# Performance work log

Hardware: AMD Instinct MI355X
Metric: run time of the kernel (lower is better)

Reference implementation:

```python
import jax, jax.numpy as jnp
import numpy as np

DIM_IN = 1024
DIM_K = 64
EPS = 1e-5

def setup_inputs() -> dict:
    key = jax.random.key(0)
    ks = jax.random.split(key, 9)
    s_in = 1.0 / np.sqrt(DIM_IN)
    s_k = 1.0 / np.sqrt(DIM_K)
    return {
        "X": jax.random.normal(ks[0], (8, 2048, DIM_IN), dtype=jnp.float32),
        "Wq": jax.random.uniform(ks[1], (DIM_IN, DIM_K), jnp.float32, -s_in, s_in),
        "bq": jax.random.uniform(ks[2], (DIM_K,), jnp.float32, -s_in, s_in),
        "Wk": jax.random.uniform(ks[3], (DIM_IN, DIM_K), jnp.float32, -s_in, s_in),
        "bk": jax.random.uniform(ks[4], (DIM_K,), jnp.float32, -s_in, s_in),
        "Wv": jax.random.uniform(ks[5], (DIM_IN, DIM_K), jnp.float32, -s_in, s_in),
        "bv": jax.random.uniform(ks[6], (DIM_K,), jnp.float32, -s_in, s_in),
        "Wo": jax.random.uniform(ks[7], (DIM_K, DIM_IN), jnp.float32, -s_k, s_k),
        "bo": jax.random.uniform(ks[8], (DIM_IN,), jnp.float32, -s_k, s_k),
        "gamma": jnp.ones((DIM_IN,), jnp.float32),
        "beta": jnp.zeros((DIM_IN,), jnp.float32),
    }

def reference(X, Wq, bq, Wk, bk, Wv, bv, Wo, bo, gamma, beta):
    q = X @ Wq + bq                       # [B,S,K]
    k = X @ Wk + bk
    v = X @ Wv + bv
    scores = jnp.einsum("bqk,bsk->bqs", q, k) / jnp.sqrt(jnp.float32(DIM_K))
    attn = jax.nn.softmax(scores, axis=2)  # [B,S,S]
    av = jnp.einsum("bqs,bsk->bqk", attn, v)
    y = X + av @ Wo + bo                  # residual, [B,S,D]
    mu = jnp.mean(y, axis=-1, keepdims=True)
    var = jnp.mean(jnp.square(y - mu), axis=-1, keepdims=True)
    return (y - mu) / jnp.sqrt(var + EPS) * gamma + beta
```

## Files before the change

kernel.cpp:

```cpp
#include <hip/hip_runtime.h>
#include <hip/hip_bf16.h>

#define DIM_D 1024
#define DIM_KH 64
#define SEQ   2048
#define BATCH 8
#define NROWS (BATCH*SEQ)
#define KVSPLIT 4
#define KEYS_PER_SPLIT (SEQ/KVSPLIT)

typedef __attribute__((ext_vector_type(8))) short short8;
typedef __attribute__((ext_vector_type(4))) short short4v;
typedef __attribute__((ext_vector_type(4))) float floatx4;

__device__ __forceinline__ ushort f2bf(float f) {
    union { __hip_bfloat16 h; ushort u; } cv;
    cv.h = __float2bfloat16(f);
    return cv.u;
}

__device__ __forceinline__ uint4 pack8(float4 a, float4 b) {
    uint4 p;
    p.x = (uint)f2bf(a.x) | ((uint)f2bf(a.y) << 16);
    p.y = (uint)f2bf(a.z) | ((uint)f2bf(a.w) << 16);
    p.z = (uint)f2bf(b.x) | ((uint)f2bf(b.y) << 16);
    p.w = (uint)f2bf(b.z) | ((uint)f2bf(b.w) << 16);
    return p;
}

__global__ void wcvt_kernel(const float* __restrict__ Wq,
                            const float* __restrict__ Wk,
                            const float* __restrict__ Wv,
                            ushort* __restrict__ WT)
{
    const int n  = blockIdx.x;
    const int o  = n >> 6;
    const int nn = n & 63;
    const float* W = (o == 0) ? Wq : (o == 1) ? Wk : Wv;
    #pragma unroll
    for (int i = 0; i < 4; i++) {
        int k = threadIdx.x + i * 256;
        WT[(size_t)n * DIM_D + k] = f2bf(W[(size_t)k * DIM_KH + nn]);
    }
}

__global__ void wocvt_kernel(const float* __restrict__ Wo, ushort* __restrict__ WoT)
{
    const int tid = threadIdx.x;
    const int n = blockIdx.x * 4 + (tid >> 6);
    const int k = tid & 63;
    WoT[(size_t)n * DIM_KH + k] = f2bf(Wo[(size_t)k * DIM_D + n]);
}

__global__ __launch_bounds__(256, 1) void qkv_mfma(
    const float* __restrict__ X, const ushort* __restrict__ WT,
    const float* __restrict__ bq, const float* __restrict__ bk,
    const float* __restrict__ bv,
    ushort* __restrict__ Qb, ushort* __restrict__ Kb, ushort* __restrict__ Vb)
{
    const int tid = threadIdx.x;
    const int m0  = blockIdx.x * 64;
    const int o   = blockIdx.y;

    __shared__ ushort Xs[2][64 * 64];
    __shared__ ushort Wls[2][64 * 64];

    const int w  = tid >> 6;
    const int l  = tid & 63;
    const int ql = l & 15;
    const int g  = (l >> 4) & 3;
    const int swz = (ql & 7) << 3;

    const int sr  = tid >> 2;
    const int sc  = (tid & 3) << 4;
    const int ssw = (sr & 7) << 3;
    const float*  Xrow = X  + (size_t)(m0 + sr) * DIM_D + sc;
    const ushort* Wrow = WT + (size_t)(o * 64 + sr) * DIM_D + sc;

    float4 xr[4];
    uint4  wr[2];

    floatx4 acc[4];
    #pragma unroll
    for (int fn = 0; fn < 4; fn++) acc[fn] = (floatx4){0.f, 0.f, 0.f, 0.f};

    #pragma unroll
    for (int f = 0; f < 4; f++)
        xr[f] = *reinterpret_cast<const float4*>(Xrow + f * 4);
    #pragma unroll
    for (int h = 0; h < 2; h++)
        wr[h] = *reinterpret_cast<const uint4*>(Wrow + h * 8);
    #pragma unroll
    for (int h = 0; h < 2; h++) {
        *reinterpret_cast<uint4*>(&Xs[0][sr * 64 + ((sc + h * 8) ^ ssw)]) =
            pack8(xr[2 * h], xr[2 * h + 1]);
        *reinterpret_cast<uint4*>(&Wls[0][sr * 64 + ((sc + h * 8) ^ ssw)]) = wr[h];
    }
    __syncthreads();

    #pragma unroll
    for (int t = 0; t < 16; t++) {
        const int cur = t & 1;
        const int nxt = cur ^ 1;
        if (t < 15) {
            const int k1 = (t + 1) * 64;
            #pragma unroll
            for (int f = 0; f < 4; f++)
                xr[f] = *reinterpret_cast<const float4*>(Xrow + k1 + f * 4);
            #pragma unroll
            for (int h = 0; h < 2; h++)
                wr[h] = *reinterpret_cast<const uint4*>(Wrow + k1 + h * 8);
        }

        #pragma unroll
        for (int kk = 0; kk < 2; kk++) {
            short8 a = *reinterpret_cast<const short8*>(
                &Xs[cur][(16 * w + ql) * 64 + ((kk * 32 + g * 8) ^ swz)]);
            #pragma unroll
            for (int fn = 0; fn < 4; fn++) {
                short8 b = *reinterpret_cast<const short8*>(
                    &Wls[cur][(16 * fn + ql) * 64 + ((kk * 32 + g * 8) ^ swz)]);
                acc[fn] = __builtin_amdgcn_mfma_f32_16x16x32_bf16(a, b, acc[fn], 0, 0, 0);
            }
        }

        if (t < 15) {
            #pragma unroll
            for (int h = 0; h < 2; h++) {
                *reinterpret_cast<uint4*>(&Xs[nxt][sr * 64 + ((sc + h * 8) ^ ssw)]) =
                    pack8(xr[2 * h], xr[2 * h + 1]);
                *reinterpret_cast<uint4*>(&Wls[nxt][sr * 64 + ((sc + h * 8) ^ ssw)]) = wr[h];
            }
        }
        __syncthreads();
    }

    const float* bias = (o == 0) ? bq : (o == 1) ? bk : bv;
    ushort* O = (o == 0) ? Qb : (o == 1) ? Kb : Vb;
    float bvreg[4];
    #pragma unroll
    for (int fn = 0; fn < 4; fn++) bvreg[fn] = bias[16 * fn + ql];

    #pragma unroll
    for (int fn = 0; fn < 4; fn++) {
        #pragma unroll
        for (int r = 0; r < 4; r++) {
            int row = m0 + 16 * w + 4 * g + r;
            O[(size_t)row * DIM_KH + 16 * fn + ql] = f2bf(acc[fn][r] + bvreg[fn]);
        }
    }
}

__global__ __launch_bounds__(256) void attn_mfma(
    const ushort* __restrict__ Qb, const ushort* __restrict__ Kb,
    const ushort* __restrict__ Vb,
    float* __restrict__ Opart, float* __restrict__ Ml)
{
    const int tid = threadIdx.x;
    const int w   = tid >> 6;
    const int l   = tid & 63;
    const int ql  = l & 15;
    const int g   = (l >> 4) & 3;
    const int q0  = blockIdx.x * 64;
    const int s   = blockIdx.y;
    const int b   = blockIdx.z;
    const int swzq = (ql & 7) << 3;

    __shared__ ushort Ks[64 * 64];
    __shared__ ushort VTs[64 * 64];

    short8 qf[2];
    #pragma unroll
    for (int kk = 0; kk < 2; kk++) {
        qf[kk] = *reinterpret_cast<const short8*>(
            Qb + ((size_t)(b * SEQ + q0 + 16 * w + ql)) * DIM_KH + kk * 32 + g * 8);
    }

    floatx4 accv[4];
    #pragma unroll
    for (int fd = 0; fd < 4; fd++) accv[fd] = (floatx4){0.f, 0.f, 0.f, 0.f};
    float m_run = -3.0e38f, l_run = 0.f;

    const ushort* Kbb = Kb + (size_t)b * SEQ * DIM_KH;
    const ushort* Vbb = Vb + (size_t)b * SEQ * DIM_KH;
    const int t_begin = s * KEYS_PER_SPLIT;
    const int t_end   = t_begin + KEYS_PER_SPLIT;

    for (int t0 = t_begin; t0 < t_end; t0 += 64) {
        __syncthreads();
        #pragma unroll
        for (int i = 0; i < 2; i++) {
            int idx = tid + i * 256;
            int row = idx >> 3;
            int ch  = idx & 7;
            uint4 v = *reinterpret_cast<const uint4*>(
                Kbb + (size_t)(t0 + row) * DIM_KH + ch * 8);
            *reinterpret_cast<uint4*>(&Ks[row * 64 + ((ch * 8) ^ ((row & 7) << 3))]) = v;
        }
        {
            int kg = tid >> 4, dg = tid & 15;
            int key0 = kg * 4, dim0 = dg * 4;
            uint2 vr[4];
            #pragma unroll
            for (int i = 0; i < 4; i++)
                vr[i] = *reinterpret_cast<const uint2*>(
                    Vbb + (size_t)(t0 + key0 + i) * DIM_KH + dim0);
            #pragma unroll
            for (int j = 0; j < 4; j++) {
                uint e0 = (j == 0) ? (vr[0].x & 0xffffu) : (j == 1) ? (vr[0].x >> 16)
                        : (j == 2) ? (vr[0].y & 0xffffu) : (vr[0].y >> 16);
                uint e1 = (j == 0) ? (vr[1].x & 0xffffu) : (j == 1) ? (vr[1].x >> 16)
                        : (j == 2) ? (vr[1].y & 0xffffu) : (vr[1].y >> 16);
                uint e2 = (j == 0) ? (vr[2].x & 0xffffu) : (j == 1) ? (vr[2].x >> 16)
                        : (j == 2) ? (vr[2].y & 0xffffu) : (vr[2].y >> 16);
                uint e3 = (j == 0) ? (vr[3].x & 0xffffu) : (j == 1) ? (vr[3].x >> 16)
                        : (j == 2) ? (vr[3].y & 0xffffu) : (vr[3].y >> 16);
                uint2 p; p.x = e0 | (e1 << 16); p.y = e2 | (e3 << 16);
                int dim = dim0 + j;
                int addr = dim * 64 + (key0 ^ ((dim & 15) << 2));
                *reinterpret_cast<uint2*>(&VTs[addr]) = p;
            }
        }
        __syncthreads();

        floatx4 sfrag[4];
        #pragma unroll
        for (int f = 0; f < 4; f++) {
            sfrag[f] = (floatx4){0.f, 0.f, 0.f, 0.f};
            #pragma unroll
            for (int kk = 0; kk < 2; kk++) {
                short8 a = *reinterpret_cast<const short8*>(
                    &Ks[(16 * f + ql) * 64 + ((kk * 32 + g * 8) ^ swzq)]);
                sfrag[f] = __builtin_amdgcn_mfma_f32_16x16x32_bf16(a, qf[kk], sfrag[f], 0, 0, 0);
            }
        }

        float mt = -3.0e38f;
        #pragma unroll
        for (int f = 0; f < 4; f++)
            #pragma unroll
            for (int r = 0; r < 4; r++) mt = fmaxf(mt, sfrag[f][r]);
        mt = fmaxf(mt, __shfl_xor(mt, 16));
        mt = fmaxf(mt, __shfl_xor(mt, 32));
        float m_new = fmaxf(m_run, mt);
        float sc = __expf((m_run - m_new) * 0.125f);
        float psum = 0.f;
        ushort pb[4][4];
        #pragma unroll
        for (int f = 0; f < 4; f++)
            #pragma unroll
            for (int r = 0; r < 4; r++) {
                float p = __expf((sfrag[f][r] - m_new) * 0.125f);
                pb[f][r] = f2bf(p);
                psum += p;
            }
        psum += __shfl_xor(psum, 16);
        psum += __shfl_xor(psum, 32);
        l_run = l_run * sc + psum;
        m_run = m_new;

        float s0 = __shfl(sc, 4 * g + 0);
        float s1 = __shfl(sc, 4 * g + 1);
        float s2 = __shfl(sc, 4 * g + 2);
        float s3 = __shfl(sc, 4 * g + 3);
        #pragma unroll
        for (int fd = 0; fd < 4; fd++) {
            accv[fd][0] *= s0; accv[fd][1] *= s1;
            accv[fd][2] *= s2; accv[fd][3] *= s3;
        }

        short8 pa_lo, pa_hi;
        pa_lo[0] = (short)pb[0][0]; pa_lo[1] = (short)pb[0][1];
        pa_lo[2] = (short)pb[0][2]; pa_lo[3] = (short)pb[0][3];
        pa_lo[4] = (short)pb[1][0]; pa_lo[5] = (short)pb[1][1];
        pa_lo[6] = (short)pb[1][2]; pa_lo[7] = (short)pb[1][3];
        pa_hi[0] = (short)pb[2][0]; pa_hi[1] = (short)pb[2][1];
        pa_hi[2] = (short)pb[2][2]; pa_hi[3] = (short)pb[2][3];
        pa_hi[4] = (short)pb[3][0]; pa_hi[5] = (short)pb[3][1];
        pa_hi[6] = (short)pb[3][2]; pa_hi[7] = (short)pb[3][3];

        #pragma unroll
        for (int fd = 0; fd < 4; fd++) {
            int dim = 16 * fd + ql;
            int base = dim * 64;
            int sw = (dim & 15) << 2;
            short4v v0 = *reinterpret_cast<const short4v*>(&VTs[base + ((4 * g) ^ sw)]);
            short4v v1 = *reinterpret_cast<const short4v*>(&VTs[base + ((16 + 4 * g) ^ sw)]);
            short8 bb;
            bb[0] = v0[0]; bb[1] = v0[1]; bb[2] = v0[2]; bb[3] = v0[3];
            bb[4] = v1[0]; bb[5] = v1[1]; bb[6] = v1[2]; bb[7] = v1[3];
            accv[fd] = __builtin_amdgcn_mfma_f32_16x16x32_bf16(pa_lo, bb, accv[fd], 0, 0, 0);
            short4v v2 = *reinterpret_cast<const short4v*>(&VTs[base + ((32 + 4 * g) ^ sw)]);
            short4v v3 = *reinterpret_cast<const short4v*>(&VTs[base + ((48 + 4 * g) ^ sw)]);
            short8 bb2;
            bb2[0] = v2[0]; bb2[1] = v2[1]; bb2[2] = v2[2]; bb2[3] = v2[3];
            bb2[4] = v3[0]; bb2[5] = v3[1]; bb2[6] = v3[2]; bb2[7] = v3[3];
            accv[fd] = __builtin_amdgcn_mfma_f32_16x16x32_bf16(pa_hi, bb2, accv[fd], 0, 0, 0);
        }
    }

    const size_t rid0 = (size_t)b * SEQ + q0;
    if (g == 0) {
        size_t rid = rid0 + 16 * w + ql;
        Ml[((size_t)s * NROWS + rid) * 2 + 0] = m_run;
        Ml[((size_t)s * NROWS + rid) * 2 + 1] = l_run;
    }
    #pragma unroll
    for (int fd = 0; fd < 4; fd++) {
        int col = 16 * fd + ql;
        size_t rbase = (size_t)s * NROWS + rid0 + 16 * w + 4 * g;
        Opart[(rbase + 0) * DIM_KH + col] = accv[fd][0];
        Opart[(rbase + 1) * DIM_KH + col] = accv[fd][1];
        Opart[(rbase + 2) * DIM_KH + col] = accv[fd][2];
        Opart[(rbase + 3) * DIM_KH + col] = accv[fd][3];
    }
}

__global__ __launch_bounds__(256) void attn_combine(
    const float* __restrict__ Opart, const float* __restrict__ Ml,
    ushort* __restrict__ AVb)
{
    const int tid = threadIdx.x;
    const size_t rid = (size_t)blockIdx.x * 16 + (tid >> 4);
    const int d0 = (tid & 15) * 4;

    float m[KVSPLIT], lv[KVSPLIT];
    float M = -3.0e38f;
    #pragma unroll
    for (int s = 0; s < KVSPLIT; s++) {
        m[s]  = Ml[((size_t)s * NROWS + rid) * 2 + 0];
        lv[s] = Ml[((size_t)s * NROWS + rid) * 2 + 1];
        M = fmaxf(M, m[s]);
    }
    float wsum = 0.f;
    float o0 = 0.f, o1 = 0.f, o2 = 0.f, o3 = 0.f;
    #pragma unroll
    for (int s = 0; s < KVSPLIT; s++) {
        float wgt = __expf((m[s] - M) * 0.125f);
        wsum = fmaf(wgt, lv[s], wsum);
        float4 a = *reinterpret_cast<const float4*>(
            Opart + ((size_t)s * NROWS + rid) * DIM_KH + d0);
        o0 = fmaf(wgt, a.x, o0);
        o1 = fmaf(wgt, a.y, o1);
        o2 = fmaf(wgt, a.z, o2);
        o3 = fmaf(wgt, a.w, o3);
    }
    float inv = 1.0f / wsum;
    uint2 p;
    p.x = (uint)f2bf(o0 * inv) | ((uint)f2bf(o1 * inv) << 16);
    p.y = (uint)f2bf(o2 * inv) | ((uint)f2bf(o3 * inv) << 16);
    *reinterpret_cast<uint2*>(AVb + rid * DIM_KH + d0) = p;
}

__global__ __launch_bounds__(256) void out_mfma(
    const float* __restrict__ X, const ushort* __restrict__ AVb,
    const ushort* __restrict__ WoT, const float* __restrict__ bo,
    const float* __restrict__ gamma, const float* __restrict__ beta,
    float* __restrict__ Out)
{
    const int tid = threadIdx.x;
    const int w   = tid >> 6;
    const int l   = tid & 63;
    const int ql  = l & 15;
    const int g   = (l >> 4) & 3;
    const int row = blockIdx.x * 16 + ql;
    const int c0  = w * 256;

    __shared__ float redS[4][16];
    __shared__ float redQ[4][16];

    short8 bf0 = *reinterpret_cast<const short8*>(AVb + (size_t)row * DIM_KH + g * 8);
    short8 bf1 = *reinterpret_cast<const short8*>(AVb + (size_t)row * DIM_KH + 32 + g * 8);

    floatx4 acc[16];
    #pragma unroll
    for (int ft = 0; ft < 16; ft++) {
        const ushort* ap = WoT + (size_t)(c0 + 16 * ft + ql) * DIM_KH + g * 8;
        short8 a0 = *reinterpret_cast<const short8*>(ap);
        short8 a1 = *reinterpret_cast<const short8*>(ap + 32);
        floatx4 z = (floatx4){0.f, 0.f, 0.f, 0.f};
        z = __builtin_amdgcn_mfma_f32_16x16x32_bf16(a0, bf0, z, 0, 0, 0);
        z = __builtin_amdgcn_mfma_f32_16x16x32_bf16(a1, bf1, z, 0, 0, 0);
        acc[ft] = z;
    }

    float s = 0.f, sq = 0.f;
    #pragma unroll
    for (int ft = 0; ft < 16; ft++) {
        int col = c0 + 16 * ft + 4 * g;
        float4 x4 = *reinterpret_cast<const float4*>(X + (size_t)row * DIM_D + col);
        float4 b4 = *reinterpret_cast<const float4*>(bo + col);
        float y0 = acc[ft][0] + x4.x + b4.x;
        float y1 = acc[ft][1] + x4.y + b4.y;
        float y2 = acc[ft][2] + x4.z + b4.z;
        float y3 = acc[ft][3] + x4.w + b4.w;
        acc[ft][0] = y0; acc[ft][1] = y1; acc[ft][2] = y2; acc[ft][3] = y3;
        s  += (y0 + y1) + (y2 + y3);
        sq += fmaf(y0, y0, fmaf(y1, y1, fmaf(y2, y2, y3 * y3)));
    }
    s  += __shfl_xor(s, 16);  s  += __shfl_xor(s, 32);
    sq += __shfl_xor(sq, 16); sq += __shfl_xor(sq, 32);
    if (l < 16) { redS[w][ql] = s; redQ[w][ql] = sq; }
    __syncthreads();
    float st = (redS[0][ql] + redS[1][ql]) + (redS[2][ql] + redS[3][ql]);
    float qt = (redQ[0][ql] + redQ[1][ql]) + (redQ[2][ql] + redQ[3][ql]);
    float mu  = st * (1.0f / 1024.0f);
    float var = fmaf(qt, (1.0f / 1024.0f), -mu * mu);
    float inv = rsqrtf(var + 1e-5f);

    #pragma unroll
    for (int ft = 0; ft < 16; ft++) {
        int col = c0 + 16 * ft + 4 * g;
        float4 g4  = *reinterpret_cast<const float4*>(gamma + col);
        float4 be4 = *reinterpret_cast<const float4*>(beta + col);
        float4 ov;
        ov.x = fmaf((acc[ft][0] - mu) * inv, g4.x, be4.x);
        ov.y = fmaf((acc[ft][1] - mu) * inv, g4.y, be4.y);
        ov.z = fmaf((acc[ft][2] - mu) * inv, g4.z, be4.z);
        ov.w = fmaf((acc[ft][3] - mu) * inv, g4.w, be4.w);
        *reinterpret_cast<float4*>(Out + (size_t)row * DIM_D + col) = ov;
    }
}

extern "C" void kernel_launch(void* const* d_in, const int* in_sizes, int n_in,
                              void* d_out, int out_size, void* d_ws, size_t ws_size,
                              hipStream_t stream)
{
    (void)in_sizes; (void)n_in; (void)out_size; (void)ws_size;
    const float* X     = (const float*)d_in[0];
    const float* Wq    = (const float*)d_in[1];
    const float* bq    = (const float*)d_in[2];
    const float* Wk    = (const float*)d_in[3];
    const float* bk    = (const float*)d_in[4];
    const float* Wv    = (const float*)d_in[5];
    const float* bv    = (const float*)d_in[6];
    const float* Wo    = (const float*)d_in[7];
    const float* bo    = (const float*)d_in[8];
    const float* gamma = (const float*)d_in[9];
    const float* beta  = (const float*)d_in[10];
    float* Out = (float*)d_out;

    ushort* Qb  = (ushort*)d_ws;
    ushort* Kb  = Qb + (size_t)NROWS * DIM_KH;
    ushort* Vb  = Kb + (size_t)NROWS * DIM_KH;
    ushort* AVb = Vb + (size_t)NROWS * DIM_KH;
    ushort* WT  = AVb + (size_t)NROWS * DIM_KH;
    ushort* WoT = WT + (size_t)192 * DIM_D;
    float*  Opart = (float*)(WoT + (size_t)DIM_D * DIM_KH);
    float*  Ml    = Opart + (size_t)KVSPLIT * NROWS * DIM_KH;

    wcvt_kernel<<<192, 256, 0, stream>>>(Wq, Wk, Wv, WT);
    wocvt_kernel<<<256, 256, 0, stream>>>(Wo, WoT);
    qkv_mfma<<<dim3(256, 3), 256, 0, stream>>>(X, WT, bq, bk, bv, Qb, Kb, Vb);
    attn_mfma<<<dim3(SEQ/64, KVSPLIT, BATCH), 256, 0, stream>>>(Qb, Kb, Vb, Opart, Ml);
    attn_combine<<<NROWS/16, 256, 0, stream>>>(Opart, Ml, AVb);
    out_mfma<<<NROWS/16, 256, 0, stream>>>(X, AVb, WoT, bo, gamma, beta, Out);
}
```

Before: 105.6 us.

## Stage out-projection tile through swizzled LDS for row-contiguous epilogue access

The output-projection kernel now writes its MFMA results into a 64KB XOR-swizzled shared-memory tile, then reassigns threads so 16 lanes cover one row with contiguous float4 columns. Reads of X and writes of Out become row-contiguous and coalesced, where before they were 16-byte fragments strided across rows. The LayerNorm reduction now finishes with intra-row shuffles instead of a cross-wave LDS reduction. The cost is 64KB of LDS per block, which limits occupancy (launch bounds set to 1), plus an extra barrier and an LDS round trip.

```diff
diff --git a/kernel.cpp b/kernel.cpp
--- a/kernel.cpp
+++ b/kernel.cpp
@@ -352,7 +352,7 @@
     *reinterpret_cast<uint2*>(AVb + rid * DIM_KH + d0) = p;
 }
 
-__global__ __launch_bounds__(256) void out_mfma(
+__global__ __launch_bounds__(256, 1) void out_mfma(
     const float* __restrict__ X, const ushort* __restrict__ AVb,
     const ushort* __restrict__ WoT, const float* __restrict__ bo,
     const float* __restrict__ gamma, const float* __restrict__ beta,
@@ -363,16 +363,14 @@
     const int l   = tid & 63;
     const int ql  = l & 15;
     const int g   = (l >> 4) & 3;
-    const int row = blockIdx.x * 16 + ql;
+    const int row0 = blockIdx.x * 16;
     const int c0  = w * 256;
 
-    __shared__ float redS[4][16];
-    __shared__ float redQ[4][16];
-
-    short8 bf0 = *reinterpret_cast<const short8*>(AVb + (size_t)row * DIM_KH + g * 8);
-    short8 bf1 = *reinterpret_cast<const short8*>(AVb + (size_t)row * DIM_KH + 32 + g * 8);
-
-    floatx4 acc[16];
+    __shared__ float Ls[16 * 1024];
+
+    short8 bf0 = *reinterpret_cast<const short8*>(AVb + (size_t)(row0 + ql) * DIM_KH + g * 8);
+    short8 bf1 = *reinterpret_cast<const short8*>(AVb + (size_t)(row0 + ql) * DIM_KH + 32 + g * 8);
+
     #pragma unroll
     for (int ft = 0; ft < 16; ft++) {
         const ushort* ap = WoT + (size_t)(c0 + 16 * ft + ql) * DIM_KH + g * 8;
@@ -381,44 +379,53 @@
         floatx4 z = (floatx4){0.f, 0.f, 0.f, 0.f};
         z = __builtin_amdgcn_mfma_f32_16x16x32_bf16(a0, bf0, z, 0, 0, 0);
         z = __builtin_amdgcn_mfma_f32_16x16x32_bf16(a1, bf1, z, 0, 0, 0);
-        acc[ft] = z;
-    }
-
+        int col = (c0 + 16 * ft + 4 * g) ^ ((ql & 7) << 2);
+        *reinterpret_cast<floatx4*>(&Ls[ql * 1024 + col]) = z;
+    }
+    __syncthreads();
+
+    const int r  = tid >> 4;
+    const int cb = (tid & 15) * 4;
+    const int rsw = (r & 7) << 2;
+    const float* Xrow = X + (size_t)(row0 + r) * DIM_D;
+
+    float4 yv[16];
     float s = 0.f, sq = 0.f;
     #pragma unroll
-    for (int ft = 0; ft < 16; ft++) {
-        int col = c0 + 16 * ft + 4 * g;
-        float4 x4 = *reinterpret_cast<const float4*>(X + (size_t)row * DIM_D + col);
+    for (int j = 0; j < 16; j++) {
+        int col = cb + 64 * j;
+        float4 a  = *reinterpret_cast<const float4*>(&Ls[r * 1024 + (col ^ rsw)]);
+        float4 x4 = *reinterpret_cast<const float4*>(Xrow + col);
         float4 b4 = *reinterpret_cast<const float4*>(bo + col);
-        float y0 = acc[ft][0] + x4.x + b4.x;
-        float y1 = acc[ft][1] + x4.y + b4.y;
-        float y2 = acc[ft][2] + x4.z + b4.z;
-        float y3 = acc[ft][3] + x4.w + b4.w;
-        acc[ft][0] = y0; acc[ft][1] = y1; acc[ft][2] = y2; acc[ft][3] = y3;
+        float y0 = a.x + x4.x + b4.x;
+        float y1 = a.y + x4.y + b4.y;
+        float y2 = a.z + x4.z + b4.z;
+        float y3 = a.w + x4.w + b4.w;
+        yv[j] = (float4){y0, y1, y2, y3};
         s  += (y0 + y1) + (y2 + y3);
         sq += fmaf(y0, y0, fmaf(y1, y1, fmaf(y2, y2, y3 * y3)));
     }
-    s  += __shfl_xor(s, 16);  s  += __shfl_xor(s, 32);
-    sq += __shfl_xor(sq, 16); sq += __shfl_xor(sq, 32);
-    if (l < 16) { redS[w][ql] = s; redQ[w][ql] = sq; }
-    __syncthreads();
-    float st = (redS[0][ql] + redS[1][ql]) + (redS[2][ql] + redS[3][ql]);
-    float qt = (redQ[0][ql] + redQ[1][ql]) + (redQ[2][ql] + redQ[3][ql]);
-    float mu  = st * (1.0f / 1024.0f);
-    float var = fmaf(qt, (1.0f / 1024.0f), -mu * mu);
+    s  += __shfl_xor(s, 1);  s  += __shfl_xor(s, 2);
+    s  += __shfl_xor(s, 4);  s  += __shfl_xor(s, 8);
+    sq += __shfl_xor(sq, 1); sq += __shfl_xor(sq, 2);
+    sq += __shfl_xor(sq, 4); sq += __shfl_xor(sq, 8);
+
+    float mu  = s * (1.0f / 1024.0f);
+    float var = fmaf(sq, (1.0f / 1024.0f), -mu * mu);
     float inv = rsqrtf(var + 1e-5f);
 
-    #pragma unroll
-    for (int ft = 0; ft < 16; ft++) {
-        int col = c0 + 16 * ft + 4 * g;
+    float* Orow = Out + (size_t)(row0 + r) * DIM_D;
+    #pragma unroll
+    for (int j = 0; j < 16; j++) {
+        int col = cb + 64 * j;
         float4 g4  = *reinterpret_cast<const float4*>(gamma + col);
         float4 be4 = *reinterpret_cast<const float4*>(beta + col);
         float4 ov;
-        ov.x = fmaf((acc[ft][0] - mu) * inv, g4.x, be4.x);
-        ov.y = fmaf((acc[ft][1] - mu) * inv, g4.y, be4.y);
-        ov.z = fmaf((acc[ft][2] - mu) * inv, g4.z, be4.z);
-        ov.w = fmaf((acc[ft][3] - mu) * inv, g4.w, be4.w);
-        *reinterpret_cast<float4*>(Out + (size_t)row * DIM_D + col) = ov;
+        ov.x = fmaf((yv[j].x - mu) * inv, g4.x, be4.x);
+        ov.y = fmaf((yv[j].y - mu) * inv, g4.y, be4.y);
+        ov.z = fmaf((yv[j].z - mu) * inv, g4.z, be4.z);
+        ov.w = fmaf((yv[j].w - mu) * inv, g4.w, be4.w);
+        *reinterpret_cast<float4*>(Orow + col) = ov;
     }
 }
 
```

After: 98.18 us. -7.1%, faster.
